# Optimization experiments

Measured on AMD Instinct MI355X. Metric: run time of the kernel, lower is better.

The kernel has to match this reference:

```python
import jax, jax.numpy as jnp
import numpy as np

N_QUBITS = 8
N_LAYERS = 2
DIM = 2 ** N_QUBITS  # 256
SBERT_DIM = 768
BATCH = 65536

# PauliZ sign table: wire 0 is the most-significant bit (PennyLane convention).
_idx = np.arange(DIM)
_bits = (_idx[None, :] >> (N_QUBITS - 1 - np.arange(N_QUBITS))[:, None]) & 1
_SIGNS = (1.0 - 2.0 * _bits).astype(np.float32)  # [N_QUBITS, DIM]


def _apply_ry(state, theta, q):
    """Apply RY(theta) on qubit q. state: [B, 2]*8; theta: [B] or scalar.
    RY is real, so the statevector stays real-valued throughout."""
    c = jnp.cos(theta * 0.5)
    s = jnp.sin(theta * 0.5)
    if jnp.ndim(c) == 1:  # per-sample angles -> broadcast over qubit axes
        bshape = (c.shape[0],) + (1,) * (N_QUBITS - 1)
        c = c.reshape(bshape)
        s = s.reshape(bshape)
    s0 = jnp.take(state, 0, axis=q + 1)
    s1 = jnp.take(state, 1, axis=q + 1)
    return jnp.stack([c * s0 - s * s1, s * s0 + c * s1], axis=q + 1)


def _apply_cnot(state, ctrl, tgt):
    """CNOT with control=ctrl, target=tgt (tgt > ctrl here)."""
    a0 = jnp.take(state, 0, axis=ctrl + 1)
    a1 = jnp.take(state, 1, axis=ctrl + 1)
    # target axis index after removing the control axis
    t_ax = tgt if tgt > ctrl else tgt + 1
    a1 = jnp.flip(a1, axis=t_ax)  # flip target amplitude when control=1
    return jnp.stack([a0, a1], axis=ctrl + 1)


def _circuit(angles, weights):
    """Batched 8-qubit statevector simulation. angles: [B, 8]; weights: [2, 8].
    Returns <Z_i> for each wire: [B, 8]."""
    B = angles.shape[0]
    state = jnp.zeros((B, DIM), angles.dtype).at[:, 0].set(1.0)
    state = state.reshape((B,) + (2,) * N_QUBITS)
    for q in range(N_QUBITS):
        state = _apply_ry(state, angles[:, q], q)
    for layer in range(N_LAYERS):
        for q in range(N_QUBITS):
            state = _apply_ry(state, weights[layer, q], q)
        for q in range(N_QUBITS - 1):
            state = _apply_cnot(state, q, q + 1)
    probs = (state * state).reshape(B, DIM)
    return probs @ jnp.asarray(_SIGNS, dtype=probs.dtype).T  # [B, 8]


def setup_inputs() -> dict:
    key = jax.random.key(0)
    k_x, k_w, k_q = jax.random.split(key, 3)
    x = jax.random.normal(k_x, (BATCH, SBERT_DIM), dtype=jnp.float32)
    W_proj = jax.random.normal(k_w, (N_QUBITS, SBERT_DIM), dtype=jnp.float32) * (1.0 / np.sqrt(SBERT_DIM))
    scale = jnp.asarray(np.pi / 2.0, dtype=jnp.float32)
    weights = 0.01 * jax.random.normal(k_q, (N_LAYERS, N_QUBITS), dtype=jnp.float32)
    return {"x": x, "W_proj": W_proj, "scale": scale, "weights": weights}


def reference(x, W_proj, scale, weights):
    h = jnp.tanh(x @ W_proj.T) * scale  # [B, 8]
    return _circuit(h, weights).astype(jnp.float32)
```

## Files before the change

### kernel.cpp

```cpp
#include <hip/hip_runtime.h>


__device__ __forceinline__ float fast_tanh(float v) {
    float e = __expf(2.0f * v);
    return 1.0f - 2.0f / (e + 1.0f);
}

__global__ __launch_bounds__(256, 3)
void pqc_kernel(const float* __restrict__ x,
                const float* __restrict__ Wp,
                const float* __restrict__ scalep,
                const float* __restrict__ wts,
                float* __restrict__ out)
{
    __shared__ float hb[64][8];

    const int tid  = threadIdx.x;
    const int lane = tid & 63;
    const int wave = tid >> 6;
    const int b0   = blockIdx.x * 64;

    const int s4  = lane >> 4;
    const int c16 = lane & 15;

    const int rbase = b0 + wave * 16;
    float acc[4][8];
    #pragma unroll
    for (int p = 0; p < 4; ++p)
        #pragma unroll
        for (int q = 0; q < 8; ++q) acc[p][q] = 0.0f;

    #pragma unroll 2
    for (int j = 0; j < 12; ++j) {
        const int col4 = j * 16 + c16;
        float4 wv[8];
        #pragma unroll
        for (int q = 0; q < 8; ++q)
            wv[q] = *reinterpret_cast<const float4*>(Wp + q * 768 + col4 * 4);
        #pragma unroll
        for (int p = 0; p < 4; ++p) {
            const float4 xv = *reinterpret_cast<const float4*>(
                x + (size_t)(rbase + p * 4 + s4) * 768 + col4 * 4);
            #pragma unroll
            for (int q = 0; q < 8; ++q) {
                acc[p][q] = fmaf(xv.x, wv[q].x, acc[p][q]);
                acc[p][q] = fmaf(xv.y, wv[q].y, acc[p][q]);
                acc[p][q] = fmaf(xv.z, wv[q].z, acc[p][q]);
                acc[p][q] = fmaf(xv.w, wv[q].w, acc[p][q]);
            }
        }
    }
    #pragma unroll
    for (int m = 1; m <= 8; m <<= 1)
        #pragma unroll
        for (int p = 0; p < 4; ++p)
            #pragma unroll
            for (int q = 0; q < 8; ++q)
                acc[p][q] += __shfl_xor(acc[p][q], m, 64);

    if (c16 == 0) {
        #pragma unroll
        for (int p = 0; p < 4; ++p) {
            const int srow = wave * 16 + p * 4 + s4;
            #pragma unroll
            for (int q = 0; q < 8; ++q) hb[srow][q] = acc[p][q];
        }
    }
    __syncthreads();

    if (lane < 16) {
        const int sl   = wave * 16 + lane;
        const int samp = b0 + sl;
        const float scl = scalep[0];

        float f0[8], f1[8];
        #pragma unroll
        for (int q = 0; q < 8; ++q) {
            float ang = fast_tanh(hb[sl][q]) * scl + wts[q];
            __sincosf(0.5f * ang, &f1[q], &f0[q]);
        }
        float c2[8], s2[8], cs[8];
        #pragma unroll
        for (int q = 0; q < 8; ++q) {
            float sw, cw;
            __sincosf(0.5f * wts[8 + q], &sw, &cw);
            c2[q] = cw * cw; s2[q] = sw * sw; cs[q] = cw * sw;
        }

        float Lp[9][2][3];
        Lp[0][0][0] = 1.f; Lp[0][0][1] = 0.f; Lp[0][0][2] = 0.f;
        Lp[0][1][0] = 0.f; Lp[0][1][1] = 0.f; Lp[0][1][2] = 0.f;

        #pragma unroll
        for (int q = 0; q < 8; ++q) {
            const float A = f0[q] * f0[q];
            const float B = f0[q] * f1[q];
            const float C = f1[q] * f1[q];
            float u[2][3];
            #pragma unroll
            for (int b = 0; b < 2; ++b) {
                const float v0 = Lp[q][b][0], v1 = Lp[q][b][1], v2 = Lp[q][b][2];
                u[b][0] = A * v0 + 2.f * B * v1 + C * v2;
                u[b][1] = B * v0 + (A + C) * v1 + B * v2;
                u[b][2] = C * v0 + 2.f * B * v1 + A * v2;
            }
            Lp[q+1][0][0] = c2[q] * u[0][0] + s2[q] * u[1][0];
            Lp[q+1][1][0] = s2[q] * u[0][0] + c2[q] * u[1][0];
            const float m = cs[q] * (u[1][1] - u[0][1]);
            Lp[q+1][0][1] = m;
            Lp[q+1][1][1] = -m;
            Lp[q+1][0][2] = s2[q] * u[0][2] + c2[q] * u[1][2];
            Lp[q+1][1][2] = c2[q] * u[0][2] + s2[q] * u[1][2];
        }

        float S[2][3] = {{1.f, 1.f, 1.f}, {1.f, 1.f, 1.f}};
        float z[8];
        #pragma unroll
        for (int i = 7; i >= 0; --i) {
            z[i] = (S[0][0] * Lp[i+1][0][0] + 2.f * S[0][1] * Lp[i+1][0][1] + S[0][2] * Lp[i+1][0][2])
                 - (S[1][0] * Lp[i+1][1][0] + 2.f * S[1][1] * Lp[i+1][1][1] + S[1][2] * Lp[i+1][1][2]);
            if (i > 0) {
                float u[2][3];
                u[0][0] = c2[i] * S[0][0] + s2[i] * S[1][0];
                u[1][0] = s2[i] * S[0][0] + c2[i] * S[1][0];
                const float m = cs[i] * (S[1][1] - S[0][1]);
                u[0][1] = m; u[1][1] = -m;
                u[0][2] = s2[i] * S[0][2] + c2[i] * S[1][2];
                u[1][2] = c2[i] * S[0][2] + s2[i] * S[1][2];
                const float A = f0[i] * f0[i];
                const float B = f0[i] * f1[i];
                const float C = f1[i] * f1[i];
                #pragma unroll
                for (int b = 0; b < 2; ++b) {
                    const float u0 = u[b][0], u1 = u[b][1], u2 = u[b][2];
                    S[b][0] = A * u0 + 2.f * B * u1 + C * u2;
                    S[b][1] = B * u0 + (A + C) * u1 + B * u2;
                    S[b][2] = C * u0 + 2.f * B * u1 + A * u2;
                }
            }
        }

        float4* o = reinterpret_cast<float4*>(out + (size_t)samp * 8);
        o[0] = make_float4(z[0], z[1], z[2], z[3]);
        o[1] = make_float4(z[4], z[5], z[6], z[7]);
    }
}

extern "C" void kernel_launch(void* const* d_in, const int* in_sizes, int n_in,
                              void* d_out, int out_size, void* d_ws, size_t ws_size,
                              hipStream_t stream) {
    const float* x   = (const float*)d_in[0];
    const float* W   = (const float*)d_in[1];
    const float* sc  = (const float*)d_in[2];
    const float* wt  = (const float*)d_in[3];
    float* o         = (float*)d_out;

    const int batch  = in_sizes[0] / 768;
    const int blocks = batch / 64;
    pqc_kernel<<<dim3(blocks), dim3(256), 0, stream>>>(x, W, sc, wt, o);
}
```

Measured before the change: 43.44 us.

## Prefetch x tiles in registers and compute circuit epilogue per lane without LDS

The projection loop now software-pipelines the x loads: the next column tile is loaded into registers while FMAs run on the current one, and the loop is no longer unrolled. Each 16-lane group owns four contiguous rows. After the xor-reduction every lane selects its own row's sums, which removes the shared-memory staging and the __syncthreads. The quantum-circuit epilogue runs redundantly across lanes and only one lane per row writes the output. Launch bounds are raised to 4 blocks per CU for more occupancy, at the cost of register pressure from the extra prefetch buffers.

```diff
diff --git a/kernel.cpp b/kernel.cpp
--- a/kernel.cpp
+++ b/kernel.cpp
@@ -6,50 +6,60 @@
     return 1.0f - 2.0f / (e + 1.0f);
 }
 
-__global__ __launch_bounds__(256, 3)
+__global__ __launch_bounds__(256, 4)
 void pqc_kernel(const float* __restrict__ x,
                 const float* __restrict__ Wp,
                 const float* __restrict__ scalep,
                 const float* __restrict__ wts,
                 float* __restrict__ out)
 {
-    __shared__ float hb[64][8];
-
-    const int tid  = threadIdx.x;
-    const int lane = tid & 63;
-    const int wave = tid >> 6;
-    const int b0   = blockIdx.x * 64;
+    const int tid   = threadIdx.x;
+    const int lane  = tid & 63;
+    const int wave  = tid >> 6;
+    const int rbase = blockIdx.x * 64 + wave * 16;
 
     const int s4  = lane >> 4;
     const int c16 = lane & 15;
 
-    const int rbase = b0 + wave * 16;
+    const float* xrow = x + (size_t)(rbase + s4 * 4) * 768 + c16 * 4;
+
     float acc[4][8];
     #pragma unroll
     for (int p = 0; p < 4; ++p)
         #pragma unroll
         for (int q = 0; q < 8; ++q) acc[p][q] = 0.0f;
 
-    #pragma unroll 2
+    float4 xv[4], xn[4];
+    #pragma unroll
+    for (int p = 0; p < 4; ++p)
+        xv[p] = *reinterpret_cast<const float4*>(xrow + p * 768);
+
+    #pragma unroll 1
     for (int j = 0; j < 12; ++j) {
-        const int col4 = j * 16 + c16;
         float4 wv[8];
+        const float* wcol = Wp + j * 64 + c16 * 4;
         #pragma unroll
         for (int q = 0; q < 8; ++q)
-            wv[q] = *reinterpret_cast<const float4*>(Wp + q * 768 + col4 * 4);
+            wv[q] = *reinterpret_cast<const float4*>(wcol + q * 768);
+        if (j < 11) {
+            const float* xcol = xrow + (j + 1) * 64;
+            #pragma unroll
+            for (int p = 0; p < 4; ++p)
+                xn[p] = *reinterpret_cast<const float4*>(xcol + p * 768);
+        }
         #pragma unroll
-        for (int p = 0; p < 4; ++p) {
-            const float4 xv = *reinterpret_cast<const float4*>(
-                x + (size_t)(rbase + p * 4 + s4) * 768 + col4 * 4);
+        for (int p = 0; p < 4; ++p)
             #pragma unroll
             for (int q = 0; q < 8; ++q) {
-                acc[p][q] = fmaf(xv.x, wv[q].x, acc[p][q]);
-                acc[p][q] = fmaf(xv.y, wv[q].y, acc[p][q]);
-                acc[p][q] = fmaf(xv.z, wv[q].z, acc[p][q]);
-                acc[p][q] = fmaf(xv.w, wv[q].w, acc[p][q]);
+                acc[p][q] = fmaf(xv[p].x, wv[q].x, acc[p][q]);
+                acc[p][q] = fmaf(xv[p].y, wv[q].y, acc[p][q]);
+                acc[p][q] = fmaf(xv[p].z, wv[q].z, acc[p][q]);
+                acc[p][q] = fmaf(xv[p].w, wv[q].w, acc[p][q]);
             }
-        }
+        #pragma unroll
+        for (int p = 0; p < 4; ++p) xv[p] = xn[p];
     }
+
     #pragma unroll
     for (int m = 1; m <= 8; m <<= 1)
         #pragma unroll
@@ -58,88 +68,86 @@
             for (int q = 0; q < 8; ++q)
                 acc[p][q] += __shfl_xor(acc[p][q], m, 64);
 
-    if (c16 == 0) {
+    const bool b0 = (lane & 1) != 0;
+    const bool b1 = (lane & 2) != 0;
+    float h[8];
+    #pragma unroll
+    for (int q = 0; q < 8; ++q) {
+        const float v01 = b0 ? acc[1][q] : acc[0][q];
+        const float v23 = b0 ? acc[3][q] : acc[2][q];
+        h[q] = b1 ? v23 : v01;
+    }
+    const int samp = rbase + s4 * 4 + (lane & 3);
+
+    const float scl = scalep[0];
+    float f0[8], f1[8];
+    #pragma unroll
+    for (int q = 0; q < 8; ++q) {
+        float ang = fast_tanh(h[q]) * scl + wts[q];
+        __sincosf(0.5f * ang, &f1[q], &f0[q]);
+    }
+    float c2[8], s2[8], cs[8];
+    #pragma unroll
+    for (int q = 0; q < 8; ++q) {
+        float sw, cw;
+        __sincosf(0.5f * wts[8 + q], &sw, &cw);
+        c2[q] = cw * cw; s2[q] = sw * sw; cs[q] = cw * sw;
+    }
+
+    float Lp[9][2][3];
+    Lp[0][0][0] = 1.f; Lp[0][0][1] = 0.f; Lp[0][0][2] = 0.f;
+    Lp[0][1][0] = 0.f; Lp[0][1][1] = 0.f; Lp[0][1][2] = 0.f;
+
+    #pragma unroll
+    for (int q = 0; q < 8; ++q) {
+        const float A = f0[q] * f0[q];
+        const float B = f0[q] * f1[q];
+        const float C = f1[q] * f1[q];
+        float u[2][3];
         #pragma unroll
-        for (int p = 0; p < 4; ++p) {
-            const int srow = wave * 16 + p * 4 + s4;
+        for (int b = 0; b < 2; ++b) {
+            const float v0 = Lp[q][b][0], v1 = Lp[q][b][1], v2 = Lp[q][b][2];
+            u[b][0] = A * v0 + 2.f * B * v1 + C * v2;
+            u[b][1] = B * v0 + (A + C) * v1 + B * v2;
+            u[b][2] = C * v0 + 2.f * B * v1 + A * v2;
+        }
+        Lp[q+1][0][0] = c2[q] * u[0][0] + s2[q] * u[1][0];
+        Lp[q+1][1][0] = s2[q] * u[0][0] + c2[q] * u[1][0];
+        const float m = cs[q] * (u[1][1] - u[0][1]);
+        Lp[q+1][0][1] = m;
+        Lp[q+1][1][1] = -m;
+        Lp[q+1][0][2] = s2[q] * u[0][2] + c2[q] * u[1][2];
+        Lp[q+1][1][2] = c2[q] * u[0][2] + s2[q] * u[1][2];
+    }
+
+    float S[2][3] = {{1.f, 1.f, 1.f}, {1.f, 1.f, 1.f}};
+    float z[8];
+    #pragma unroll
+    for (int i = 7; i >= 0; --i) {
+        z[i] = (S[0][0] * Lp[i+1][0][0] + 2.f * S[0][1] * Lp[i+1][0][1] + S[0][2] * Lp[i+1][0][2])
+             - (S[1][0] * Lp[i+1][1][0] + 2.f * S[1][1] * Lp[i+1][1][1] + S[1][2] * Lp[i+1][1][2]);
+        if (i > 0) {
+            float u[2][3];
+            u[0][0] = c2[i] * S[0][0] + s2[i] * S[1][0];
+            u[1][0] = s2[i] * S[0][0] + c2[i] * S[1][0];
+            const float m = cs[i] * (S[1][1] - S[0][1]);
+            u[0][1] = m; u[1][1] = -m;
+            u[0][2] = s2[i] * S[0][2] + c2[i] * S[1][2];
+            u[1][2] = c2[i] * S[0][2] + s2[i] * S[1][2];
+            const float A = f0[i] * f0[i];
+            const float B = f0[i] * f1[i];
+            const float C = f1[i] * f1[i];
             #pragma unroll
-            for (int q = 0; q < 8; ++q) hb[srow][q] = acc[p][q];
+            for (int b = 0; b < 2; ++b) {
+                const float u0 = u[b][0], u1 = u[b][1], u2 = u[b][2];
+                S[b][0] = A * u0 + 2.f * B * u1 + C * u2;
+                S[b][1] = B * u0 + (A + C) * u1 + B * u2;
+                S[b][2] = C * u0 + 2.f * B * u1 + A * u2;
+            }
         }
     }
-    __syncthreads();
 
-    if (lane < 16) {
-        const int sl   = wave * 16 + lane;
-        const int samp = b0 + sl;
-        const float scl = scalep[0];
-
-        float f0[8], f1[8];
-        #pragma unroll
-        for (int q = 0; q < 8; ++q) {
-            float ang = fast_tanh(hb[sl][q]) * scl + wts[q];
-            __sincosf(0.5f * ang, &f1[q], &f0[q]);
-        }
-        float c2[8], s2[8], cs[8];
-        #pragma unroll
-        for (int q = 0; q < 8; ++q) {
-            float sw, cw;
-            __sincosf(0.5f * wts[8 + q], &sw, &cw);
-            c2[q] = cw * cw; s2[q] = sw * sw; cs[q] = cw * sw;
-        }
-
-        float Lp[9][2][3];
-        Lp[0][0][0] = 1.f; Lp[0][0][1] = 0.f; Lp[0][0][2] = 0.f;
-        Lp[0][1][0] = 0.f; Lp[0][1][1] = 0.f; Lp[0][1][2] = 0.f;
-
-        #pragma unroll
-        for (int q = 0; q < 8; ++q) {
-            const float A = f0[q] * f0[q];
-            const float B = f0[q] * f1[q];
-            const float C = f1[q] * f1[q];
-            float u[2][3];
-            #pragma unroll
-            for (int b = 0; b < 2; ++b) {
-                const float v0 = Lp[q][b][0], v1 = Lp[q][b][1], v2 = Lp[q][b][2];
-                u[b][0] = A * v0 + 2.f * B * v1 + C * v2;
-                u[b][1] = B * v0 + (A + C) * v1 + B * v2;
-                u[b][2] = C * v0 + 2.f * B * v1 + A * v2;
-            }
-            Lp[q+1][0][0] = c2[q] * u[0][0] + s2[q] * u[1][0];
-            Lp[q+1][1][0] = s2[q] * u[0][0] + c2[q] * u[1][0];
-            const float m = cs[q] * (u[1][1] - u[0][1]);
-            Lp[q+1][0][1] = m;
-            Lp[q+1][1][1] = -m;
-            Lp[q+1][0][2] = s2[q] * u[0][2] + c2[q] * u[1][2];
-            Lp[q+1][1][2] = c2[q] * u[0][2] + s2[q] * u[1][2];
-        }
-
-        float S[2][3] = {{1.f, 1.f, 1.f}, {1.f, 1.f, 1.f}};
-        float z[8];
-        #pragma unroll
-        for (int i = 7; i >= 0; --i) {
-            z[i] = (S[0][0] * Lp[i+1][0][0] + 2.f * S[0][1] * Lp[i+1][0][1] + S[0][2] * Lp[i+1][0][2])
-                 - (S[1][0] * Lp[i+1][1][0] + 2.f * S[1][1] * Lp[i+1][1][1] + S[1][2] * Lp[i+1][1][2]);
-            if (i > 0) {
-                float u[2][3];
-                u[0][0] = c2[i] * S[0][0] + s2[i] * S[1][0];
-                u[1][0] = s2[i] * S[0][0] + c2[i] * S[1][0];
-                const float m = cs[i] * (S[1][1] - S[0][1]);
-                u[0][1] = m; u[1][1] = -m;
-                u[0][2] = s2[i] * S[0][2] + c2[i] * S[1][2];
-                u[1][2] = c2[i] * S[0][2] + s2[i] * S[1][2];
-                const float A = f0[i] * f0[i];
-                const float B = f0[i] * f1[i];
-                const float C = f1[i] * f1[i];
-                #pragma unroll
-                for (int b = 0; b < 2; ++b) {
-                    const float u0 = u[b][0], u1 = u[b][1], u2 = u[b][2];
-                    S[b][0] = A * u0 + 2.f * B * u1 + C * u2;
-                    S[b][1] = B * u0 + (A + C) * u1 + B * u2;
-                    S[b][2] = C * u0 + 2.f * B * u1 + A * u2;
-                }
-            }
-        }
-
+    if ((lane & 12) == 0) {
         float4* o = reinterpret_cast<float4*>(out + (size_t)samp * 8);
         o[0] = make_float4(z[0], z[1], z[2], z[3]);
         o[1] = make_float4(z[4], z[5], z[6], z[7]);
```

Measured after the change: 70.97 us. +63.4%, slower.
